# Performance work log

Hardware: AMD Instinct MI355X
Metric: run time of the kernel (lower is better)

## Reference

```python
import jax, jax.numpy as jnp
import numpy as np

GROUPSIZE = 128
ZERO_POINT = 8  # (maxq + 1) // 2 with maxq = 2**4 - 1


def setup_inputs() -> dict:
    key = jax.random.key(0)
    kA, ks, kq = jax.random.split(key, 3)
    M, K, N = 4096, 4096, 4096
    A = jax.random.normal(kA, (M, K), dtype=jnp.float32)
    # per-group scales, positive and small like real quantization scales
    s = jax.random.uniform(ks, (K // GROUPSIZE, N), dtype=jnp.float32) * 0.02 + 1e-3
    # int4 weights in [0, 15], packed 8 nibbles per int32 word along n
    nib = jax.random.randint(kq, (K, N), 0, 16, dtype=jnp.int32).astype(jnp.uint32)
    shifts = (4 * jnp.arange(8, dtype=jnp.uint32))
    q_u = (nib.reshape(K, N // 8, 8) << shifts).sum(axis=-1)  # uint32 (K, N//8)
    q = jax.lax.bitcast_convert_type(q_u, jnp.int32)
    return {"A": A, "s": s, "q": q}


def reference(A, s, q):
    # Unpack 8 int4 nibbles per int32 word: (K, N//8) -> (K, N)
    shifts = 4 * jnp.arange(8, dtype=jnp.int32)
    nib = (q[:, :, None] >> shifts) & 0xF  # (K, N//8, 8)
    nib = nib.reshape(q.shape[0], -1)      # (K, N)
    # Symmetric dequant with zero-point 8 and per-group (groupsize=128 rows) scales
    w = (nib.astype(A.dtype) - ZERO_POINT) * jnp.repeat(s.astype(A.dtype), GROUPSIZE, axis=0)
    return A @ w  # (M, N)
```

## Files before the change

### kernel.cpp

```cpp
#include <hip/hip_runtime.h>
#include <stdint.h>

#define GM 4096
#define GN 4096
#define GK 4096
#define QW (GN/8)

typedef __attribute__((ext_vector_type(4))) int   i32x4;
typedef __attribute__((ext_vector_type(8))) short bf16x8;
typedef __attribute__((ext_vector_type(4))) float f32x4;

#define AS1 __attribute__((address_space(1)))
#define AS3 __attribute__((address_space(3)))

static __device__ __forceinline__ void glds16(const void* g, void* l) {
  __builtin_amdgcn_global_load_lds((const AS1 uint32_t*)g, (AS3 uint32_t*)l, 16, 0, 0);
}

static __device__ __forceinline__ uint32_t bf16pack_rn(float hi, float lo) {
  uint32_t h = __float_as_uint(hi) + 0x8000u;
  uint32_t l = __float_as_uint(lo) + 0x8000u;
  return __builtin_amdgcn_perm(h, l, 0x07060302u);
}

static __device__ __forceinline__ uint32_t pack4i8(int b0, int b1, int b2, int b3) {
  return ((uint32_t)b0 & 255u) | (((uint32_t)b1 & 255u) << 8) |
         (((uint32_t)b2 & 255u) << 16) | (((uint32_t)b3 & 255u) << 24);
}

__global__ void __launch_bounds__(256) a_quant(const float* __restrict__ A,
                                               int8_t* __restrict__ Ai,
                                               float* __restrict__ ascale) {
  const int t    = threadIdx.x;
  const int lane = t & 63;
  const int row  = blockIdx.x * 4 + (t >> 6);
  const float* src = A + (size_t)row * GK;
  float4 v[16];
  float m = 0.f;
  #pragma unroll
  for (int i = 0; i < 16; ++i) {
    v[i] = *(const float4*)(src + i * 256 + lane * 4);
    m = fmaxf(m, fmaxf(fmaxf(fabsf(v[i].x), fabsf(v[i].y)),
                       fmaxf(fabsf(v[i].z), fabsf(v[i].w))));
  }
  #pragma unroll
  for (int off = 32; off >= 1; off >>= 1)
    m = fmaxf(m, __shfl_xor(m, off, 64));
  const float rmax = fmaxf(m, 1e-20f);
  const float inv  = 127.0f / rmax;
  #pragma unroll
  for (int i = 0; i < 16; ++i) {
    uint32_t b = pack4i8((int)__builtin_rintf(v[i].x * inv),
                         (int)__builtin_rintf(v[i].y * inv),
                         (int)__builtin_rintf(v[i].z * inv),
                         (int)__builtin_rintf(v[i].w * inv));
    *(uint32_t*)(Ai + (size_t)row * GK + i * 256 + lane * 4) = b;
  }
  if (lane == 0) ascale[row] = rmax * (1.0f / 127.0f);
}

__global__ void __launch_bounds__(256) w_scale(const float* __restrict__ S,
                                               float* __restrict__ wscale,
                                               float* __restrict__ winv) {
  const int n = blockIdx.x * 256 + threadIdx.x;
  float m = 0.f;
  #pragma unroll 8
  for (int g = 0; g < 32; ++g) m = fmaxf(m, S[(size_t)g * GN + n]);
  wscale[n] = m * (8.0f / 127.0f);
  winv[n]   = 127.0f / (8.0f * m);
}

__global__ void __launch_bounds__(256) w_quant(const float* __restrict__ S,
                                               const uint32_t* __restrict__ Q,
                                               const float* __restrict__ winv,
                                               int8_t* __restrict__ Wt) {
  __shared__ uint32_t T32[128 * 32];
  const int tid = threadIdx.x;
  const int n0  = blockIdx.x * 128;
  const int k0  = blockIdx.y * 128;
  const int g   = blockIdx.y;
  const int w   = tid & 15;
  const int kb  = tid >> 4;

  float r[8], c[8];
  {
    const float* sp = S + (size_t)g * GN + n0 + w * 8;
    const float* ip = winv + n0 + w * 8;
    float4 sa = *(const float4*)sp, sb = *(const float4*)(sp + 4);
    float4 ia = *(const float4*)ip, ib = *(const float4*)(ip + 4);
    const float sv[8] = {sa.x, sa.y, sa.z, sa.w, sb.x, sb.y, sb.z, sb.w};
    const float iv[8] = {ia.x, ia.y, ia.z, ia.w, ib.x, ib.y, ib.z, ib.w};
    #pragma unroll
    for (int j = 0; j < 8; ++j) { r[j] = sv[j] * iv[j]; c[j] = -8.0f * r[j]; }
  }

  const int swz = 4 * (w & 7);
  #pragma unroll
  for (int c2 = 0; c2 < 2; ++c2) {
    uint32_t q[4];
    #pragma unroll
    for (int i = 0; i < 4; ++i)
      q[i] = Q[(size_t)(k0 + c2 * 64 + kb * 4 + i) * QW + (n0 >> 3) + w];
    const int kword = c2 * 16 + kb;
    #pragma unroll
    for (int j = 0; j < 8; ++j) {
      int b[4];
      #pragma unroll
      for (int i = 0; i < 4; ++i) {
        float nib = (float)((q[i] >> (4 * j)) & 0xFu);
        b[i] = (int)__builtin_rintf(fmaf(nib, r[j], c[j]));
      }
      T32[(w * 8 + j) * 32 + (kword ^ swz)] = pack4i8(b[0], b[1], b[2], b[3]);
    }
  }
  __syncthreads();
  #pragma unroll
  for (int p = 0; p < 4; ++p) {
    int idx = p * 256 + tid;
    int n = idx >> 3, gr = idx & 7;
    uint4 v = *(const uint4*)(&T32[n * 32 + (gr ^ ((n >> 3) & 7)) * 4]);
    *(uint4*)(Wt + (size_t)(n0 + n) * GK + k0 + gr * 16) = v;
  }
}

__global__ void __launch_bounds__(256, 4) gemm_i8(const int8_t* __restrict__ Ai,
                                                  const int8_t* __restrict__ Wi,
                                                  const float* __restrict__ ascale,
                                                  const float* __restrict__ wscale,
                                                  float* __restrict__ C) {
  __shared__ __align__(16) int8_t As[128 * 128];
  __shared__ __align__(16) int8_t Bs[128 * 128];

  const int tid  = threadIdx.x;
  const int m0   = blockIdx.y * 128;
  const int n0   = blockIdx.x * 128;
  const int ln   = tid & 63;
  const int wid  = tid >> 6;
  const int wm   = (wid >> 1) * 64;
  const int wn   = (wid & 1) * 64;
  const int col  = ln & 15;
  const int quad = ln >> 4;

  const int rs = tid >> 3;
  const int qo = ((tid & 7) ^ (rs & 7)) * 16;
  const int8_t* Asrc = Ai + (size_t)(m0 + rs) * GK + qo;
  const int8_t* Bsrc = Wi + (size_t)(n0 + rs) * GK + qo;

  const int sw = col & 7;

  i32x4 acc[4][4];
  #pragma unroll
  for (int i = 0; i < 4; ++i)
    #pragma unroll
    for (int j = 0; j < 4; ++j)
      acc[i][j] = (i32x4){0, 0, 0, 0};

  for (int k0 = 0; k0 < GK; k0 += 128) {
    #pragma unroll
    for (int c = 0; c < 4; ++c) {
      glds16(Asrc + (size_t)c * 32 * GK + k0, &As[(c * 256 + tid) * 16]);
      glds16(Bsrc + (size_t)c * 32 * GK + k0, &Bs[(c * 256 + tid) * 16]);
    }

    __syncthreads();

    #pragma unroll
    for (int kk = 0; kk < 2; ++kk) {
      const int cq = ((kk * 4 + quad) ^ sw) * 16;
      i32x4 af[4], bfr[4];
      #pragma unroll
      for (int t = 0; t < 4; ++t) {
        af[t]  = *(const i32x4*)(&As[(wm + t * 16 + col) * 128 + cq]);
        bfr[t] = *(const i32x4*)(&Bs[(wn + t * 16 + col) * 128 + cq]);
      }
      #pragma unroll
      for (int mt = 0; mt < 4; ++mt)
        #pragma unroll
        for (int nt = 0; nt < 4; ++nt)
          acc[mt][nt] = __builtin_amdgcn_mfma_i32_16x16x64_i8(
                            af[mt], bfr[nt], acc[mt][nt], 0, 0, 0);
    }

    __syncthreads();
  }

  #pragma unroll
  for (int mt = 0; mt < 4; ++mt) {
    float4 a4 = *(const float4*)(ascale + m0 + wm + mt * 16 + quad * 4);
    const float ar[4] = {a4.x, a4.y, a4.z, a4.w};
    #pragma unroll
    for (int nt = 0; nt < 4; ++nt) {
      const float ws = wscale[n0 + wn + nt * 16 + col];
      #pragma unroll
      for (int r = 0; r < 4; ++r)
        C[(size_t)(m0 + wm + mt * 16 + quad * 4 + r) * GN
          + n0 + wn + nt * 16 + col] = (float)acc[mt][nt][r] * (ar[r] * ws);
    }
  }
}

#define BM 128
#define BN 128
#define BK 32

__global__ void __launch_bounds__(256) w4a32_gemm(
    const float* __restrict__ A,
    const float* __restrict__ S,
    const uint32_t* __restrict__ Q,
    float* __restrict__ C)
{
  __shared__ __align__(16) ushort As[BM*BK];
  __shared__ __align__(16) ushort Bs[BN*BK];

  const int tid  = threadIdx.x;
  const int m0   = blockIdx.y*BM;
  const int n0   = blockIdx.x*BN;
  const int wcol  = tid & 15;
  const int kpair = tid >> 4;
  const int ln   = tid & 63;
  const int wid  = tid >> 6;
  const int wm   = (wid >> 1) * 64;
  const int wn   = (wid & 1) * 64;
  const int col  = ln & 15;
  const int quad = ln >> 4;

  f32x4 acc[4][4];
  #pragma unroll
  for (int i=0;i<4;++i)
    #pragma unroll
    for (int j=0;j<4;++j)
      acc[i][j] = (f32x4){0.f,0.f,0.f,0.f};

  float sv[8], cv[8];
  float4 spf0, spf1;

  const float*    Abase = A + (size_t)m0 * GK;
  const uint32_t* Qbase = Q + (size_t)(n0>>3) + wcol;

  {
    const float* sp = S + n0 + wcol*8;
    spf0 = *(const float4*)sp;
    spf1 = *(const float4*)(sp + 4);
  }

  float4 a4[4];
  uint32_t wqa, wqb;
  #pragma unroll
  for (int i=0;i<4;++i) {
    int f = tid + i*256;
    a4[i] = *(const float4*)(Abase + (size_t)(f>>3)*GK + ((f&7)*4));
  }
  wqa = Qbase[(size_t)(2*kpair)   * QW];
  wqb = Qbase[(size_t)(2*kpair+1) * QW];

  for (int k0 = 0; k0 < GK; k0 += BK) {
    if ((k0 & 127) == 0) {
      sv[0]=spf0.x; sv[1]=spf0.y; sv[2]=spf0.z; sv[3]=spf0.w;
      sv[4]=spf1.x; sv[5]=spf1.y; sv[6]=spf1.z; sv[7]=spf1.w;
      #pragma unroll
      for (int j=0;j<8;++j) cv[j] = -8.0f * sv[j];
    }

    #pragma unroll
    for (int i=0;i<4;++i) {
      int f = tid + i*256;
      int row = f>>3, c4 = f&7;
      *(uint2*)(&As[row*BK + c4*4]) =
        make_uint2(bf16pack_rn(a4[i].y, a4[i].x), bf16pack_rn(a4[i].w, a4[i].z));
    }

    {
      const int kk = (2*kpair) ^ (8*(wcol&3));
      #pragma unroll
      for (int j=0;j<8;++j) {
        float fa = (float)((wqa >> (4*j)) & 0xFu);
        float fb = (float)((wqb >> (4*j)) & 0xFu);
        float wa = fmaf(fa, sv[j], cv[j]);
        float wb = fmaf(fb, sv[j], cv[j]);
        int n = wcol*8 + j;
        *(uint32_t*)(&Bs[n*BK + kk]) = bf16pack_rn(wb, wa);
      }
    }

    int kn = k0 + BK; if (kn >= GK) kn = 0;
    if ((kn & 127) == 0) {
      const float* sp = S + (size_t)(kn>>7)*GN + n0 + wcol*8;
      spf0 = *(const float4*)sp;
      spf1 = *(const float4*)(sp + 4);
    }
    #pragma unroll
    for (int i=0;i<4;++i) {
      int f = tid + i*256;
      a4[i] = *(const float4*)(Abase + (size_t)(f>>3)*GK + kn + ((f&7)*4));
    }
    wqa = Qbase[(size_t)(kn + 2*kpair)   * QW];
    wqb = Qbase[(size_t)(kn + 2*kpair+1) * QW];

    __syncthreads();

    bf16x8 af[4], bfr[4];
    #pragma unroll
    for (int t=0;t<4;++t) {
      af[t] = *(const bf16x8*)(&As[(wm + t*16 + col)*BK + quad*8]);
      int n = wn + t*16 + col;
      int kk = (quad*8) ^ (8*((n>>3)&3));
      bfr[t] = *(const bf16x8*)(&Bs[n*BK + kk]);
    }
    #pragma unroll
    for (int mt=0;mt<4;++mt)
      #pragma unroll
      for (int nt=0;nt<4;++nt)
        acc[mt][nt] = __builtin_amdgcn_mfma_f32_16x16x32_bf16(
                          af[mt], bfr[nt], acc[mt][nt], 0, 0, 0);

    __syncthreads();
  }

  #pragma unroll
  for (int mt=0;mt<4;++mt)
    #pragma unroll
    for (int nt=0;nt<4;++nt)
      #pragma unroll
      for (int r=0;r<4;++r)
        C[(size_t)(m0 + wm + mt*16 + quad*4 + r)*GN + n0 + wn + nt*16 + col]
          = acc[mt][nt][r];
}

extern "C" void kernel_launch(void* const* d_in, const int* in_sizes, int n_in,
                              void* d_out, int out_size, void* d_ws, size_t ws_size,
                              hipStream_t stream) {
  const float*    A = (const float*)d_in[0];
  const float*    S = (const float*)d_in[1];
  const uint32_t* Q = (const uint32_t*)d_in[2];
  float*          C = (float*)d_out;

  const size_t need = (size_t)GM * GK + (size_t)GN * GK + 3 * 4096 * 4 + 4096;
  if (ws_size >= need) {
    int8_t* Ai  = (int8_t*)d_ws;
    int8_t* Wt  = Ai + (size_t)GM * GK;
    float* ascale = (float*)(Wt + (size_t)GN * GK);
    float* wscale = ascale + 4096;
    float* winv   = wscale + 4096;
    a_quant<<<dim3(GM / 4), dim3(256), 0, stream>>>(A, Ai, ascale);
    w_scale<<<dim3(GN / 256), dim3(256), 0, stream>>>(S, wscale, winv);
    w_quant<<<dim3(GN / 128, GK / 128), dim3(256), 0, stream>>>(S, Q, winv, Wt);
    gemm_i8<<<dim3(GN / 128, GM / 128), dim3(256), 0, stream>>>(Ai, Wt, ascale, wscale, C);
  } else {
    w4a32_gemm<<<dim3(GN / BN, GM / BM), dim3(256), 0, stream>>>(A, S, Q, C);
  }
}
```

Baseline: 212.5 us.

## Rewrite int8 GEMM as 256x256 double-buffered pipelined kernel with block swizzle

The int8 MFMA GEMM now uses 256x256 output tiles with 512 threads, and its A and B tiles are double-buffered in LDS (128 KB total). Global-to-LDS loads for later k-steps are interleaved with MFMA quadrants using fine-grained barriers, vmcnt waits and s_setprio. A block-index swizzle groups neighbouring tiles to improve L2 reuse. The aim is to hide global load latency and raise arithmetic intensity per LDS byte, at the cost of lower occupancy, heavy register use for 32 accumulators per thread, and a fragile hand-tuned wait schedule.

```diff
diff --git a/kernel.cpp b/kernel.cpp
--- a/kernel.cpp
+++ b/kernel.cpp
@@ -123,80 +123,170 @@
   }
 }
 
-__global__ void __launch_bounds__(256, 4) gemm_i8(const int8_t* __restrict__ Ai,
+__global__ void __launch_bounds__(512, 2) gemm_i8(const int8_t* __restrict__ Ai,
                                                   const int8_t* __restrict__ Wi,
                                                   const float* __restrict__ ascale,
                                                   const float* __restrict__ wscale,
                                                   float* __restrict__ C) {
-  __shared__ __align__(16) int8_t As[128 * 128];
-  __shared__ __align__(16) int8_t Bs[128 * 128];
-
-  const int tid  = threadIdx.x;
-  const int m0   = blockIdx.y * 128;
-  const int n0   = blockIdx.x * 128;
-  const int ln   = tid & 63;
+  __shared__ __align__(16) int8_t As[2][256 * 128];
+  __shared__ __align__(16) int8_t Bs[2][256 * 128];
+
+  const int tid = threadIdx.x;
+  const int bid = blockIdx.y * gridDim.x + blockIdx.x;
+  const int swb = ((bid & 7) << 5) | (bid >> 3);
+  const int m0  = (swb >> 4) * 256;
+  const int n0  = (swb & 15) * 256;
+
+  const int lane = tid & 63;
   const int wid  = tid >> 6;
-  const int wm   = (wid >> 1) * 64;
-  const int wn   = (wid & 1) * 64;
-  const int col  = ln & 15;
-  const int quad = ln >> 4;
-
-  const int rs = tid >> 3;
-  const int qo = ((tid & 7) ^ (rs & 7)) * 16;
-  const int8_t* Asrc = Ai + (size_t)(m0 + rs) * GK + qo;
-  const int8_t* Bsrc = Wi + (size_t)(n0 + rs) * GK + qo;
-
-  const int sw = col & 7;
-
-  i32x4 acc[4][4];
-  #pragma unroll
-  for (int i = 0; i < 4; ++i)
+  const int wm   = wid >> 2;
+  const int wn   = wid & 3;
+  const int col  = lane & 15;
+  const int quad = lane >> 4;
+  const int sw   = col & 7;
+
+  const int ur0   = tid >> 3;
+  const int pc    = tid & 7;
+  const int qo    = ((pc ^ (ur0 & 7)) << 4);
+  const int arow0 = ur0;
+  const int brow0 = (ur0 & 31) + ((ur0 & 32) << 1);
+  const size_t aoff = (size_t)(m0 + arow0) * GK + qo;
+  const size_t boff = (size_t)(n0 + brow0) * GK + qo;
+  const int dA0 = arow0 * 128 + pc * 16;
+  const int dB0 = brow0 * 128 + pc * 16;
+
+#define STAGE_A(b, kt, hi) do {                                              \
+    const int8_t* s_ = Ai + aoff + (size_t)(hi) * 64 * GK + (size_t)(kt) * 128; \
+    glds16(s_,                   &As[b][dA0 + (hi) * 8192]);                 \
+    glds16(s_ + (size_t)128 * GK, &As[b][dA0 + (hi) * 8192 + 16384]);        \
+  } while (0)
+#define STAGE_B(b, kt, hi) do {                                              \
+    const int8_t* s_ = Wi + boff + (size_t)(hi) * 32 * GK + (size_t)(kt) * 128; \
+    glds16(s_,                   &Bs[b][dB0 + (hi) * 4096]);                 \
+    glds16(s_ + (size_t)128 * GK, &Bs[b][dB0 + (hi) * 4096 + 16384]);        \
+  } while (0)
+
+  const int cq0 = ((quad    ) ^ sw) << 4;
+  const int cq1 = ((quad + 4) ^ sw) << 4;
+  const int aRd = (wm * 128 + col) * 128;
+  const int bRd = (wn * 64  + col) * 128;
+
+  i32x4 af[4][2], bf0[2][2], bf1[2][2];
+  i32x4 acc[8][4];
+  #pragma unroll
+  for (int i = 0; i < 8; ++i)
     #pragma unroll
     for (int j = 0; j < 4; ++j)
       acc[i][j] = (i32x4){0, 0, 0, 0};
 
-  for (int k0 = 0; k0 < GK; k0 += 128) {
-    #pragma unroll
-    for (int c = 0; c < 4; ++c) {
-      glds16(Asrc + (size_t)c * 32 * GK + k0, &As[(c * 256 + tid) * 16]);
-      glds16(Bsrc + (size_t)c * 32 * GK + k0, &Bs[(c * 256 + tid) * 16]);
-    }
-
-    __syncthreads();
-
-    #pragma unroll
-    for (int kk = 0; kk < 2; ++kk) {
-      const int cq = ((kk * 4 + quad) ^ sw) * 16;
-      i32x4 af[4], bfr[4];
-      #pragma unroll
-      for (int t = 0; t < 4; ++t) {
-        af[t]  = *(const i32x4*)(&As[(wm + t * 16 + col) * 128 + cq]);
-        bfr[t] = *(const i32x4*)(&Bs[(wn + t * 16 + col) * 128 + cq]);
-      }
-      #pragma unroll
-      for (int mt = 0; mt < 4; ++mt)
+#define LDA_(b, h) do {                                                      \
+    _Pragma("unroll")                                                        \
+    for (int m_ = 0; m_ < 4; ++m_) {                                         \
+      af[m_][0] = *(const i32x4*)(&As[b][aRd + (h) * 8192 + m_ * 2048 + cq0]); \
+      af[m_][1] = *(const i32x4*)(&As[b][aRd + (h) * 8192 + m_ * 2048 + cq1]); \
+    }                                                                        \
+  } while (0)
+#define LDB_(b, g, BF) do {                                                  \
+    _Pragma("unroll")                                                        \
+    for (int n_ = 0; n_ < 2; ++n_) {                                         \
+      BF[n_][0] = *(const i32x4*)(&Bs[b][bRd + (g) * 4096 + n_ * 2048 + cq0]); \
+      BF[n_][1] = *(const i32x4*)(&Bs[b][bRd + (g) * 4096 + n_ * 2048 + cq1]); \
+    }                                                                        \
+  } while (0)
+#define MFMAQ_(h, g, BF) do {                                                \
+    _Pragma("unroll")                                                        \
+    for (int m_ = 0; m_ < 4; ++m_)                                           \
+      _Pragma("unroll")                                                      \
+      for (int n_ = 0; n_ < 2; ++n_) {                                       \
+        acc[(h)*4+m_][(g)*2+n_] = __builtin_amdgcn_mfma_i32_16x16x64_i8(     \
+            af[m_][0], BF[n_][0], acc[(h)*4+m_][(g)*2+n_], 0, 0, 0);         \
+        acc[(h)*4+m_][(g)*2+n_] = __builtin_amdgcn_mfma_i32_16x16x64_i8(     \
+            af[m_][1], BF[n_][1], acc[(h)*4+m_][(g)*2+n_], 0, 0, 0);         \
+      }                                                                      \
+  } while (0)
+#define BAR()   __builtin_amdgcn_s_barrier()
+#define LGKM0() asm volatile("s_waitcnt lgkmcnt(0)" ::: "memory")
+#define VM6()   asm volatile("s_waitcnt vmcnt(6)" ::: "memory")
+
+  STAGE_A(0, 0, 0); STAGE_A(0, 0, 1); STAGE_B(0, 0, 0); STAGE_B(0, 0, 1);
+  STAGE_A(1, 1, 0); STAGE_B(1, 1, 0); STAGE_B(1, 1, 1);
+  VM6();
+  BAR();
+
+  for (int it = 0; it < GK / 256; ++it) {
+    const int t1 = 2 * it + 1;
+    const int t2 = (2 * it + 2) & 31;
+    const int t3 = (2 * it + 3) & 31;
+
+    LDA_(0, 0); LDB_(0, 0, bf0);
+    STAGE_A(1, t1, 1);
+    BAR(); LGKM0();
+    __builtin_amdgcn_s_setprio(1); MFMAQ_(0, 0, bf0); __builtin_amdgcn_s_setprio(0);
+    BAR();
+    LDB_(0, 1, bf1);
+    STAGE_A(0, t2, 0);
+    BAR(); LGKM0();
+    __builtin_amdgcn_s_setprio(1); MFMAQ_(0, 1, bf1); __builtin_amdgcn_s_setprio(0);
+    BAR();
+    LDA_(0, 1);
+    STAGE_B(0, t2, 0);
+    BAR(); LGKM0();
+    __builtin_amdgcn_s_setprio(1); MFMAQ_(1, 1, bf1); __builtin_amdgcn_s_setprio(0);
+    BAR();
+    STAGE_B(0, t2, 1);
+    BAR(); LGKM0();
+    __builtin_amdgcn_s_setprio(1); MFMAQ_(1, 0, bf0); __builtin_amdgcn_s_setprio(0);
+    VM6();
+    BAR();
+    LDA_(1, 0); LDB_(1, 0, bf0);
+    STAGE_A(0, t2, 1);
+    BAR(); LGKM0();
+    __builtin_amdgcn_s_setprio(1); MFMAQ_(0, 0, bf0); __builtin_amdgcn_s_setprio(0);
+    BAR();
+    LDB_(1, 1, bf1);
+    STAGE_A(1, t3, 0);
+    BAR(); LGKM0();
+    __builtin_amdgcn_s_setprio(1); MFMAQ_(0, 1, bf1); __builtin_amdgcn_s_setprio(0);
+    BAR();
+    LDA_(1, 1);
+    STAGE_B(1, t3, 0);
+    BAR(); LGKM0();
+    __builtin_amdgcn_s_setprio(1); MFMAQ_(1, 1, bf1); __builtin_amdgcn_s_setprio(0);
+    BAR();
+    STAGE_B(1, t3, 1);
+    BAR(); LGKM0();
+    __builtin_amdgcn_s_setprio(1); MFMAQ_(1, 0, bf0); __builtin_amdgcn_s_setprio(0);
+    VM6();
+    BAR();
+  }
+
+  #pragma unroll
+  for (int h = 0; h < 2; ++h)
+    #pragma unroll
+    for (int m = 0; m < 4; ++m) {
+      const int rbase = m0 + wm * 128 + h * 64 + m * 16 + quad * 4;
+      float4 a4 = *(const float4*)(ascale + rbase);
+      const float ar[4] = {a4.x, a4.y, a4.z, a4.w};
+      #pragma unroll
+      for (int g = 0; g < 2; ++g)
         #pragma unroll
-        for (int nt = 0; nt < 4; ++nt)
-          acc[mt][nt] = __builtin_amdgcn_mfma_i32_16x16x64_i8(
-                            af[mt], bfr[nt], acc[mt][nt], 0, 0, 0);
-    }
-
-    __syncthreads();
-  }
-
-  #pragma unroll
-  for (int mt = 0; mt < 4; ++mt) {
-    float4 a4 = *(const float4*)(ascale + m0 + wm + mt * 16 + quad * 4);
-    const float ar[4] = {a4.x, a4.y, a4.z, a4.w};
-    #pragma unroll
-    for (int nt = 0; nt < 4; ++nt) {
-      const float ws = wscale[n0 + wn + nt * 16 + col];
-      #pragma unroll
-      for (int r = 0; r < 4; ++r)
-        C[(size_t)(m0 + wm + mt * 16 + quad * 4 + r) * GN
-          + n0 + wn + nt * 16 + col] = (float)acc[mt][nt][r] * (ar[r] * ws);
-    }
-  }
+        for (int n = 0; n < 2; ++n) {
+          const int cbase = n0 + wn * 64 + g * 32 + n * 16 + col;
+          const float ws = wscale[cbase];
+          #pragma unroll
+          for (int r = 0; r < 4; ++r)
+            C[(size_t)(rbase + r) * GN + cbase]
+              = (float)acc[h * 4 + m][g * 2 + n][r] * (ar[r] * ws);
+        }
+    }
+#undef STAGE_A
+#undef STAGE_B
+#undef LDA_
+#undef LDB_
+#undef MFMAQ_
+#undef BAR
+#undef LGKM0
+#undef VM6
 }
 
 #define BM 128
@@ -344,7 +434,7 @@
     a_quant<<<dim3(GM / 4), dim3(256), 0, stream>>>(A, Ai, ascale);
     w_scale<<<dim3(GN / 256), dim3(256), 0, stream>>>(S, wscale, winv);
     w_quant<<<dim3(GN / 128, GK / 128), dim3(256), 0, stream>>>(S, Q, winv, Wt);
-    gemm_i8<<<dim3(GN / 128, GM / 128), dim3(256), 0, stream>>>(Ai, Wt, ascale, wscale, C);
+    gemm_i8<<<dim3(GN / 256, GM / 256), dim3(512), 0, stream>>>(Ai, Wt, ascale, wscale, C);
   } else {
     w4a32_gemm<<<dim3(GN / BN, GM / BM), dim3(256), 0, stream>>>(A, S, Q, C);
   }
```

New measurement: 193.1 us. 9.1% less time.
